# Kernel optimization log

Hardware: AMD Instinct MI355X
Metric: run time of the kernel (lower is better)

## Reference

```python
import jax, jax.numpy as jnp
import numpy as np

DIM = 384
HEAD_DIM = 32
NUM_HEADS = DIM // HEAD_DIM
SCALE = HEAD_DIM ** -0.5


def setup_inputs() -> dict:
    key = jax.random.key(0)
    k1, k2, k3, k4 = jax.random.split(key, 4)
    x = jax.random.normal(k1, (8, DIM, 32, 32), dtype=jnp.float32)
    # torch nn.Linear stores weight as [out_features, in_features]
    W_qkv = jax.random.normal(k2, (3 * DIM, DIM), dtype=jnp.float32) * (DIM ** -0.5)
    W_proj = jax.random.normal(k3, (DIM, DIM), dtype=jnp.float32) * (DIM ** -0.5)
    b_proj = jax.random.normal(k4, (DIM,), dtype=jnp.float32) * 0.01
    return {"x": x, "W_qkv": W_qkv, "W_proj": W_proj, "b_proj": b_proj}


def reference(x, W_qkv, W_proj, b_proj):
    B, C, H, W = x.shape
    N = H * W
    # flatten spatial -> tokens: (B, N, C)
    xt = x.reshape(B, C, N).transpose(0, 2, 1)
    # qkv projection (no bias): (B, N, 3C)
    qkv = jnp.einsum('bnc,oc->bno', xt, W_qkv)
    qkv = qkv.reshape(B, N, 3, NUM_HEADS, HEAD_DIM).transpose(2, 0, 3, 1, 4)
    q, k, v = qkv[0], qkv[1], qkv[2]  # each (B, h, N, d)
    attn = jnp.einsum('bhnd,bhmd->bhnm', q * SCALE, k)  # (B, h, N, N)
    attn = jax.nn.softmax(attn, axis=-1)
    out = jnp.einsum('bhnm,bhmd->bhnd', attn, v)  # (B, h, N, d)
    out = out.transpose(0, 2, 1, 3).reshape(B, N, C)
    out = jnp.einsum('bnc,oc->bno', out, W_proj) + b_proj
    # back to (B, C, H, W)
    return out.transpose(0, 2, 1).reshape(B, C, H, W)
```

## Files before the change

### kernel.cpp

```cpp
#include <hip/hip_runtime.h>
#include <hip/hip_bf16.h>

#define DIM   384
#define HD    32
#define NH    12
#define NT    1024
#define BATCH 8
#define C2 0.2550347244197545f
#define M2 11.541560327111707f


typedef short shortx8 __attribute__((ext_vector_type(8)));
typedef float floatx4 __attribute__((ext_vector_type(4)));

#define GLD_LDS(gp, lp) \
    __builtin_amdgcn_global_load_lds((__attribute__((address_space(1))) const void*)(gp), \
                                     (__attribute__((address_space(3))) void*)(lp), 16, 0, 0)

static __device__ __forceinline__ unsigned short f2bf(float f) {
    unsigned int u = __float_as_uint(f);
    u += 0x7fffu + ((u >> 16) & 1u);
    return (unsigned short)(u >> 16);
}

__global__ __launch_bounds__(256) void k_pre(const float* __restrict__ x,
                                             const float* __restrict__ wq,
                                             const float* __restrict__ wp,
                                             unsigned short* __restrict__ xtf,
                                             unsigned short* __restrict__ wqf,
                                             unsigned short* __restrict__ wpf) {
    const int bid = blockIdx.x;
    if (bid < 3072) {
        __shared__ float t[32][33];
        const int xb_ = bid & 31, kstep = (bid >> 5) % 12, b = bid / 384;
        const int n0 = xb_ * 32;
        const int tid = threadIdx.x;
        const int tx = tid & 31, ty = tid >> 5;
        const float* xb = x + ((size_t)b * DIM + kstep * 32) * NT + n0;
#pragma unroll
        for (int i = 0; i < 4; i++)
            t[ty + 8 * i][tx] = xb[(size_t)(ty + 8 * i) * NT + tx];
        __syncthreads();
        const int mtl = tid >> 7, kq = (tid >> 5) & 3, rem = tid & 31;
        const int mrow = rem >> 1, krH = rem & 1;
        ushort4 p;
        p.x = f2bf(t[kq * 8 + krH * 4 + 0][mtl * 16 + mrow]);
        p.y = f2bf(t[kq * 8 + krH * 4 + 1][mtl * 16 + mrow]);
        p.z = f2bf(t[kq * 8 + krH * 4 + 2][mtl * 16 + mrow]);
        p.w = f2bf(t[kq * 8 + krH * 4 + 3][mtl * 16 + mrow]);
        const size_t mtile = ((size_t)b * 1024 + n0) / 16 + mtl;
        const size_t off = ((mtile * 12 + kstep) * 4 + kq) * 128 + mrow * 8 + krH * 4;
        *(ushort4*)(xtf + off) = p;
    } else {
        const int tid = (bid - 3072) * 256 + threadIdx.x;
        const float* src; unsigned short* dst; int ci;
        if (tid < 110592) { ci = tid; src = wq; dst = wqf; }
        else              { ci = tid - 110592; src = wp; dst = wpf; }
        const int krH = ci & 1, orow = (ci >> 1) & 15, quad = (ci >> 5) & 3;
        const int t2 = ci >> 7, kstep = t2 % 12, ntile = t2 / 12;
        const int row = ntile * 16 + orow, col = kstep * 32 + quad * 8 + krH * 4;
        const float4 v = *(const float4*)(src + (size_t)row * DIM + col);
        ushort4 p;
        p.x = f2bf(v.x); p.y = f2bf(v.y); p.z = f2bf(v.z); p.w = f2bf(v.w);
        *(ushort4*)(dst + (size_t)ci * 4) = p;
    }
}

__global__ __launch_bounds__(256) void k_qkv(const unsigned short* __restrict__ xtf,
                                             const unsigned short* __restrict__ wqf,
                                             unsigned short* __restrict__ qb,
                                             unsigned short* __restrict__ kb,
                                             unsigned short* __restrict__ vt) {
    const int lane = threadIdx.x & 63, w = threadIdx.x >> 6;
    const int quad = lane >> 4, l16 = lane & 15;
    const int m0 = blockIdx.x * 128 + (w & 1) * 64;
    const int n0 = blockIdx.y * 128 + (w >> 1) * 64;
    floatx4 acc[4][4] = {};
    const unsigned short* abase = xtf + ((size_t)(m0 >> 4) * 12 * 4 + quad) * 128 + l16 * 8;
    const unsigned short* bbase = wqf + ((size_t)(n0 >> 4) * 12 * 4 + quad) * 128 + l16 * 8;
    shortx8 a[4], b[4], a2[4], b2[4];
#pragma unroll
    for (int s = 0; s < 4; s++) {
        a[s] = *(const shortx8*)(abase + s * 6144);
        b[s] = *(const shortx8*)(bbase + s * 6144);
    }
    for (int ks = 0; ks < 12; ks++) {
        if (ks < 11) {
#pragma unroll
            for (int s = 0; s < 4; s++) {
                a2[s] = *(const shortx8*)(abase + s * 6144 + (ks + 1) * 512);
                b2[s] = *(const shortx8*)(bbase + s * 6144 + (ks + 1) * 512);
            }
        }
#pragma unroll
        for (int sm = 0; sm < 4; sm++)
#pragma unroll
            for (int sn = 0; sn < 4; sn++)
                acc[sm][sn] = __builtin_amdgcn_mfma_f32_16x16x32_bf16(a[sm], b[sn], acc[sm][sn], 0, 0, 0);
#pragma unroll
        for (int s = 0; s < 4; s++) { a[s] = a2[s]; b[s] = b2[s]; }
    }
    const int bi = m0 >> 10;
#pragma unroll
    for (int sn = 0; sn < 4; sn++) {
        const int o = n0 + sn * 16 + l16;
        const int which = (o >= 2 * DIM) ? 2 : (o >= DIM ? 1 : 0);
        const int rem = o - which * DIM;
        const int h = rem >> 5, d = rem & 31;
        const int hi = bi * NH + h;
#pragma unroll
        for (int sm = 0; sm < 4; sm++) {
#pragma unroll
            for (int r = 0; r < 4; r++) {
                const int n = (m0 + sm * 16 + quad * 4 + r) & 1023;
                const unsigned short val = f2bf(acc[sm][sn][r]);
                if (which == 0)      qb[((size_t)hi * NT + n) * HD + d] = val;
                else if (which == 1) kb[((size_t)hi * NT + n) * HD + d] = val;
                else                 vt[((size_t)hi * HD + d) * NT + n] = val;
            }
        }
    }
}

__global__ __launch_bounds__(256) void k_attn(const unsigned short* __restrict__ qb,
                                              const unsigned short* __restrict__ kb,
                                              const unsigned short* __restrict__ vt,
                                              unsigned short* __restrict__ aoutf) {
    __shared__ __align__(16) unsigned short frag[2][4][512];
    const int lane = threadIdx.x & 63, w = threadIdx.x >> 6;
    const int quad = lane >> 4, l16 = lane & 15;
    const int g = blockIdx.x & 7, j = blockIdx.x >> 3;
    const int hi = g * 12 + j % 12;
    const int q0 = ((j / 12) * 4 + w) * 32;
    const unsigned short* Q = qb + (size_t)hi * NT * HD;
    const unsigned short* K = kb + (size_t)hi * NT * HD;
    const unsigned short* V = vt + (size_t)hi * HD * NT;

    const shortx8 qfA = *(const shortx8*)(Q + (size_t)(q0 + l16) * HD + quad * 8);
    const shortx8 qfB = *(const shortx8*)(Q + (size_t)(q0 + 16 + l16) * HD + quad * 8);
    const int krow = (l16 >> 2) * 8 + (l16 & 3);
    const unsigned short* gsrc0;
    if (w == 0)      gsrc0 = K + (size_t)krow * HD + quad * 8;
    else if (w == 1) gsrc0 = K + (size_t)(krow + 4) * HD + quad * 8;
    else if (w == 2) gsrc0 = V + (size_t)l16 * NT + quad * 8;
    else             gsrc0 = V + (size_t)(16 + l16) * NT + quad * 8;
    const int gstep = (w < 2) ? 32 * HD : 32;

    const shortx8 ones = {16256, 16256, 16256, 16256, 16256, 16256, 16256, 16256};
    floatx4 oloA = {}, ohiA = {}, dsA = {};
    floatx4 oloB = {}, ohiB = {}, dsB = {};
    const floatx4 zero = {};

    GLD_LDS(gsrc0, &frag[0][w][0]);
    __syncthreads();

    for (int t = 0; t < 32; t++) {
        if (t < 31) GLD_LDS(gsrc0 + (size_t)(t + 1) * gstep, &frag[(t + 1) & 1][w][0]);
        const unsigned short* fb = &frag[t & 1][0][0];
        const shortx8 kf0 = *(const shortx8*)(fb + 0 * 512 + lane * 8);
        const shortx8 kf1 = *(const shortx8*)(fb + 1 * 512 + lane * 8);
        const shortx8 vlo = *(const shortx8*)(fb + 2 * 512 + lane * 8);
        const shortx8 vhi = *(const shortx8*)(fb + 3 * 512 + lane * 8);
        const floatx4 sA0 = __builtin_amdgcn_mfma_f32_16x16x32_bf16(kf0, qfA, zero, 0, 0, 0);
        const floatx4 sA1 = __builtin_amdgcn_mfma_f32_16x16x32_bf16(kf1, qfA, zero, 0, 0, 0);
        const floatx4 sB0 = __builtin_amdgcn_mfma_f32_16x16x32_bf16(kf0, qfB, zero, 0, 0, 0);
        const floatx4 sB1 = __builtin_amdgcn_mfma_f32_16x16x32_bf16(kf1, qfB, zero, 0, 0, 0);
        float eA[8], eB[8];
#pragma unroll
        for (int r = 0; r < 4; r++) {
            eA[r]     = __builtin_amdgcn_exp2f(fmaf(sA0[r], C2, -M2));
            eA[4 + r] = __builtin_amdgcn_exp2f(fmaf(sA1[r], C2, -M2));
            eB[r]     = __builtin_amdgcn_exp2f(fmaf(sB0[r], C2, -M2));
            eB[4 + r] = __builtin_amdgcn_exp2f(fmaf(sB1[r], C2, -M2));
        }
        union { shortx8 s8; __hip_bfloat162 h[4]; } pA, pB;
#pragma unroll
        for (int i = 0; i < 4; i++) {
            pA.h[i] = __float22bfloat162_rn(make_float2(eA[2 * i], eA[2 * i + 1]));
            pB.h[i] = __float22bfloat162_rn(make_float2(eB[2 * i], eB[2 * i + 1]));
        }
        oloA = __builtin_amdgcn_mfma_f32_16x16x32_bf16(pA.s8, vlo, oloA, 0, 0, 0);
        ohiA = __builtin_amdgcn_mfma_f32_16x16x32_bf16(pA.s8, vhi, ohiA, 0, 0, 0);
        dsA  = __builtin_amdgcn_mfma_f32_16x16x32_bf16(pA.s8, ones, dsA, 0, 0, 0);
        oloB = __builtin_amdgcn_mfma_f32_16x16x32_bf16(pB.s8, vlo, oloB, 0, 0, 0);
        ohiB = __builtin_amdgcn_mfma_f32_16x16x32_bf16(pB.s8, vhi, ohiB, 0, 0, 0);
        dsB  = __builtin_amdgcn_mfma_f32_16x16x32_bf16(pB.s8, ones, dsB, 0, 0, 0);
        __syncthreads();
    }
    const int bi = hi / NH, h = hi % NH;
    const size_t mt0 = (size_t)bi * 64 + (q0 >> 4);
    const int kqlo = l16 >> 3, kr = l16 & 7;
    unsigned short* pAp = aoutf + (mt0 * 12 + h) * 512 + kr;
    unsigned short* pBp = aoutf + ((mt0 + 1) * 12 + h) * 512 + kr;
#pragma unroll
    for (int r = 0; r < 4; r++) {
        const int mrow8 = (quad * 4 + r) * 8;
        const float invA = 1.0f / dsA[r], invB = 1.0f / dsB[r];
        pAp[kqlo * 128 + mrow8]       = f2bf(oloA[r] * invA);
        pAp[(2 + kqlo) * 128 + mrow8] = f2bf(ohiA[r] * invA);
        pBp[kqlo * 128 + mrow8]       = f2bf(oloB[r] * invB);
        pBp[(2 + kqlo) * 128 + mrow8] = f2bf(ohiB[r] * invB);
    }
}

__global__ __launch_bounds__(256) void k_proj(const unsigned short* __restrict__ aoutf,
                                              const unsigned short* __restrict__ wpf,
                                              const float* __restrict__ bias,
                                              float* __restrict__ out) {
    const int lane = threadIdx.x & 63, w = threadIdx.x >> 6;
    const int quad = lane >> 4, l16 = lane & 15;
    const int m0 = blockIdx.x * 128 + (w & 1) * 64;
    const int n0 = blockIdx.y * 128 + (w >> 1) * 64;
    floatx4 acc[4][4] = {};
    const unsigned short* abase = aoutf + ((size_t)(m0 >> 4) * 12 * 4 + quad) * 128 + l16 * 8;
    const unsigned short* bbase = wpf + ((size_t)(n0 >> 4) * 12 * 4 + quad) * 128 + l16 * 8;
    shortx8 a[4], b[4], a2[4], b2[4];
#pragma unroll
    for (int s = 0; s < 4; s++) {
        a[s] = *(const shortx8*)(abase + s * 6144);
        b[s] = *(const shortx8*)(bbase + s * 6144);
    }
    for (int ks = 0; ks < 12; ks++) {
        if (ks < 11) {
#pragma unroll
            for (int s = 0; s < 4; s++) {
                a2[s] = *(const shortx8*)(abase + s * 6144 + (ks + 1) * 512);
                b2[s] = *(const shortx8*)(bbase + s * 6144 + (ks + 1) * 512);
            }
        }
#pragma unroll
        for (int sm = 0; sm < 4; sm++)
#pragma unroll
            for (int sn = 0; sn < 4; sn++)
                acc[sm][sn] = __builtin_amdgcn_mfma_f32_16x16x32_bf16(a[sm], b[sn], acc[sm][sn], 0, 0, 0);
#pragma unroll
        for (int s = 0; s < 4; s++) { a[s] = a2[s]; b[s] = b2[s]; }
    }
    const int bi = m0 >> 10;
#pragma unroll
    for (int sn = 0; sn < 4; sn++) {
        const int o = n0 + sn * 16 + l16;
        const float bv = bias[o];
        float* orow = out + ((size_t)bi * DIM + o) * NT;
#pragma unroll
        for (int sm = 0; sm < 4; sm++) {
            const int nb = (m0 + sm * 16 + quad * 4) & 1023;
            float4 pack;
            pack.x = acc[sm][sn][0] + bv;
            pack.y = acc[sm][sn][1] + bv;
            pack.z = acc[sm][sn][2] + bv;
            pack.w = acc[sm][sn][3] + bv;
            *(float4*)(orow + nb) = pack;
        }
    }
}

extern "C" void kernel_launch(void* const* d_in, const int* in_sizes, int n_in,
                              void* d_out, int out_size, void* d_ws, size_t ws_size,
                              hipStream_t stream) {
    const float* x     = (const float*)d_in[0];
    const float* wqkv  = (const float*)d_in[1];
    const float* wproj = (const float*)d_in[2];
    const float* bias  = (const float*)d_in[3];
    float* out = (float*)d_out;

    unsigned short* xtf  = (unsigned short*)d_ws;
    unsigned short* qb   = xtf + 3145728;
    unsigned short* kb   = qb + 3145728;
    unsigned short* vt   = kb + 3145728;
    unsigned short* wqf  = vt + 3145728;
    unsigned short* wpf  = wqf + 442368;
    unsigned short* aoutf = xtf;

    k_pre<<<3648, 256, 0, stream>>>(x, wqkv, wproj, xtf, wqf, wpf);
    k_qkv<<<dim3(64, 9), 256, 0, stream>>>(xtf, wqf, qb, kb, vt);
    k_attn<<<768, 256, 0, stream>>>(qb, kb, vt, aoutf);
    k_proj<<<dim3(64, 3), 256, 0, stream>>>(aoutf, wpf, bias, out);
}
```

Measured before the change: 128.6 us.

## Deepen GEMM prefetch, batch attention KV tiles, and retile projection grid

The QKV and projection GEMMs now prefetch two k-steps ahead using triple-buffered register fragments instead of one, and both declare a two-blocks-per-CU launch bound. The attention kernel stages eight K/V tiles per LDS phase, so it synchronises four times instead of thirty-two while keeping a double buffer. The projection kernel uses smaller 64x128 block tiles with twice as many blocks to fill more CUs. These changes aim to hide load latency and cut barrier overhead, at the cost of more registers and 64KB of LDS per attention block, which may lower occupancy.

Result: no change. 131.0 us (+1.8%).

```diff
diff --git a/kernel.cpp b/kernel.cpp
--- a/kernel.cpp
+++ b/kernel.cpp
@@ -21,6 +21,25 @@
     unsigned int u = __float_as_uint(f);
     u += 0x7fffu + ((u >> 16) & 1u);
     return (unsigned short)(u >> 16);
+}
+
+template <int NA, int NB>
+static __device__ __forceinline__ void ldfrag(shortx8 (&A)[NA], shortx8 (&B)[NB],
+                                              const unsigned short* ab,
+                                              const unsigned short* bb, int ks) {
+#pragma unroll
+    for (int s = 0; s < NA; s++) A[s] = *(const shortx8*)(ab + s * 6144 + ks * 512);
+#pragma unroll
+    for (int s = 0; s < NB; s++) B[s] = *(const shortx8*)(bb + s * 6144 + ks * 512);
+}
+template <int NA, int NB>
+static __device__ __forceinline__ void mmblk(floatx4 (&acc)[NA][NB],
+                                             const shortx8 (&A)[NA], const shortx8 (&B)[NB]) {
+#pragma unroll
+    for (int sm = 0; sm < NA; sm++)
+#pragma unroll
+        for (int sn = 0; sn < NB; sn++)
+            acc[sm][sn] = __builtin_amdgcn_mfma_f32_16x16x32_bf16(A[sm], B[sn], acc[sm][sn], 0, 0, 0);
 }
 
 __global__ __launch_bounds__(256) void k_pre(const float* __restrict__ x,
@@ -66,11 +85,11 @@
     }
 }
 
-__global__ __launch_bounds__(256) void k_qkv(const unsigned short* __restrict__ xtf,
-                                             const unsigned short* __restrict__ wqf,
-                                             unsigned short* __restrict__ qb,
-                                             unsigned short* __restrict__ kb,
-                                             unsigned short* __restrict__ vt) {
+__global__ __launch_bounds__(256, 2) void k_qkv(const unsigned short* __restrict__ xtf,
+                                                const unsigned short* __restrict__ wqf,
+                                                unsigned short* __restrict__ qb,
+                                                unsigned short* __restrict__ kb,
+                                                unsigned short* __restrict__ vt) {
     const int lane = threadIdx.x & 63, w = threadIdx.x >> 6;
     const int quad = lane >> 4, l16 = lane & 15;
     const int m0 = blockIdx.x * 128 + (w & 1) * 64;
@@ -78,27 +97,17 @@
     floatx4 acc[4][4] = {};
     const unsigned short* abase = xtf + ((size_t)(m0 >> 4) * 12 * 4 + quad) * 128 + l16 * 8;
     const unsigned short* bbase = wqf + ((size_t)(n0 >> 4) * 12 * 4 + quad) * 128 + l16 * 8;
-    shortx8 a[4], b[4], a2[4], b2[4];
-#pragma unroll
-    for (int s = 0; s < 4; s++) {
-        a[s] = *(const shortx8*)(abase + s * 6144);
-        b[s] = *(const shortx8*)(bbase + s * 6144);
-    }
-    for (int ks = 0; ks < 12; ks++) {
-        if (ks < 11) {
-#pragma unroll
-            for (int s = 0; s < 4; s++) {
-                a2[s] = *(const shortx8*)(abase + s * 6144 + (ks + 1) * 512);
-                b2[s] = *(const shortx8*)(bbase + s * 6144 + (ks + 1) * 512);
-            }
-        }
-#pragma unroll
-        for (int sm = 0; sm < 4; sm++)
-#pragma unroll
-            for (int sn = 0; sn < 4; sn++)
-                acc[sm][sn] = __builtin_amdgcn_mfma_f32_16x16x32_bf16(a[sm], b[sn], acc[sm][sn], 0, 0, 0);
-#pragma unroll
-        for (int s = 0; s < 4; s++) { a[s] = a2[s]; b[s] = b2[s]; }
+    shortx8 A0[4], B0[4], A1[4], B1[4], A2[4], B2[4];
+    ldfrag(A0, B0, abase, bbase, 0);
+    ldfrag(A1, B1, abase, bbase, 1);
+#pragma unroll
+    for (int ks = 0; ks < 12; ks += 3) {
+        if (ks + 2 < 12) ldfrag(A2, B2, abase, bbase, ks + 2);
+        mmblk(acc, A0, B0);
+        if (ks + 3 < 12) ldfrag(A0, B0, abase, bbase, ks + 3);
+        mmblk(acc, A1, B1);
+        if (ks + 4 < 12) ldfrag(A1, B1, abase, bbase, ks + 4);
+        mmblk(acc, A2, B2);
     }
     const int bi = m0 >> 10;
 #pragma unroll
@@ -126,7 +135,7 @@
                                               const unsigned short* __restrict__ kb,
                                               const unsigned short* __restrict__ vt,
                                               unsigned short* __restrict__ aoutf) {
-    __shared__ __align__(16) unsigned short frag[2][4][512];
+    __shared__ __align__(16) unsigned short frag[2][8][4][512];
     const int lane = threadIdx.x & 63, w = threadIdx.x >> 6;
     const int quad = lane >> 4, l16 = lane & 15;
     const int g = blockIdx.x & 7, j = blockIdx.x >> 3;
@@ -151,40 +160,50 @@
     floatx4 oloB = {}, ohiB = {}, dsB = {};
     const floatx4 zero = {};
 
-    GLD_LDS(gsrc0, &frag[0][w][0]);
+#pragma unroll
+    for (int t = 0; t < 8; t++)
+        GLD_LDS(gsrc0 + (size_t)t * gstep, &frag[0][t][w][0]);
     __syncthreads();
 
-    for (int t = 0; t < 32; t++) {
-        if (t < 31) GLD_LDS(gsrc0 + (size_t)(t + 1) * gstep, &frag[(t + 1) & 1][w][0]);
-        const unsigned short* fb = &frag[t & 1][0][0];
-        const shortx8 kf0 = *(const shortx8*)(fb + 0 * 512 + lane * 8);
-        const shortx8 kf1 = *(const shortx8*)(fb + 1 * 512 + lane * 8);
-        const shortx8 vlo = *(const shortx8*)(fb + 2 * 512 + lane * 8);
-        const shortx8 vhi = *(const shortx8*)(fb + 3 * 512 + lane * 8);
-        const floatx4 sA0 = __builtin_amdgcn_mfma_f32_16x16x32_bf16(kf0, qfA, zero, 0, 0, 0);
-        const floatx4 sA1 = __builtin_amdgcn_mfma_f32_16x16x32_bf16(kf1, qfA, zero, 0, 0, 0);
-        const floatx4 sB0 = __builtin_amdgcn_mfma_f32_16x16x32_bf16(kf0, qfB, zero, 0, 0, 0);
-        const floatx4 sB1 = __builtin_amdgcn_mfma_f32_16x16x32_bf16(kf1, qfB, zero, 0, 0, 0);
-        float eA[8], eB[8];
-#pragma unroll
-        for (int r = 0; r < 4; r++) {
-            eA[r]     = __builtin_amdgcn_exp2f(fmaf(sA0[r], C2, -M2));
-            eA[4 + r] = __builtin_amdgcn_exp2f(fmaf(sA1[r], C2, -M2));
-            eB[r]     = __builtin_amdgcn_exp2f(fmaf(sB0[r], C2, -M2));
-            eB[4 + r] = __builtin_amdgcn_exp2f(fmaf(sB1[r], C2, -M2));
-        }
-        union { shortx8 s8; __hip_bfloat162 h[4]; } pA, pB;
-#pragma unroll
-        for (int i = 0; i < 4; i++) {
-            pA.h[i] = __float22bfloat162_rn(make_float2(eA[2 * i], eA[2 * i + 1]));
-            pB.h[i] = __float22bfloat162_rn(make_float2(eB[2 * i], eB[2 * i + 1]));
-        }
-        oloA = __builtin_amdgcn_mfma_f32_16x16x32_bf16(pA.s8, vlo, oloA, 0, 0, 0);
-        ohiA = __builtin_amdgcn_mfma_f32_16x16x32_bf16(pA.s8, vhi, ohiA, 0, 0, 0);
-        dsA  = __builtin_amdgcn_mfma_f32_16x16x32_bf16(pA.s8, ones, dsA, 0, 0, 0);
-        oloB = __builtin_amdgcn_mfma_f32_16x16x32_bf16(pB.s8, vlo, oloB, 0, 0, 0);
-        ohiB = __builtin_amdgcn_mfma_f32_16x16x32_bf16(pB.s8, vhi, ohiB, 0, 0, 0);
-        dsB  = __builtin_amdgcn_mfma_f32_16x16x32_bf16(pB.s8, ones, dsB, 0, 0, 0);
+    for (int p = 0; p < 4; p++) {
+        const int pb = p & 1;
+        if (p < 3) {
+#pragma unroll
+            for (int t = 0; t < 8; t++)
+                GLD_LDS(gsrc0 + (size_t)((p + 1) * 8 + t) * gstep, &frag[pb ^ 1][t][w][0]);
+        }
+#pragma unroll
+        for (int t = 0; t < 8; t++) {
+            const unsigned short* fb = &frag[pb][t][0][0];
+            const shortx8 kf0 = *(const shortx8*)(fb + 0 * 512 + lane * 8);
+            const shortx8 kf1 = *(const shortx8*)(fb + 1 * 512 + lane * 8);
+            const shortx8 vlo = *(const shortx8*)(fb + 2 * 512 + lane * 8);
+            const shortx8 vhi = *(const shortx8*)(fb + 3 * 512 + lane * 8);
+            const floatx4 sA0 = __builtin_amdgcn_mfma_f32_16x16x32_bf16(kf0, qfA, zero, 0, 0, 0);
+            const floatx4 sA1 = __builtin_amdgcn_mfma_f32_16x16x32_bf16(kf1, qfA, zero, 0, 0, 0);
+            const floatx4 sB0 = __builtin_amdgcn_mfma_f32_16x16x32_bf16(kf0, qfB, zero, 0, 0, 0);
+            const floatx4 sB1 = __builtin_amdgcn_mfma_f32_16x16x32_bf16(kf1, qfB, zero, 0, 0, 0);
+            float eA[8], eB[8];
+#pragma unroll
+            for (int r = 0; r < 4; r++) {
+                eA[r]     = __builtin_amdgcn_exp2f(fmaf(sA0[r], C2, -M2));
+                eA[4 + r] = __builtin_amdgcn_exp2f(fmaf(sA1[r], C2, -M2));
+                eB[r]     = __builtin_amdgcn_exp2f(fmaf(sB0[r], C2, -M2));
+                eB[4 + r] = __builtin_amdgcn_exp2f(fmaf(sB1[r], C2, -M2));
+            }
+            union { shortx8 s8; __hip_bfloat162 h[4]; } pA, pB;
+#pragma unroll
+            for (int i = 0; i < 4; i++) {
+                pA.h[i] = __float22bfloat162_rn(make_float2(eA[2 * i], eA[2 * i + 1]));
+                pB.h[i] = __float22bfloat162_rn(make_float2(eB[2 * i], eB[2 * i + 1]));
+            }
+            oloA = __builtin_amdgcn_mfma_f32_16x16x32_bf16(pA.s8, vlo, oloA, 0, 0, 0);
+            ohiA = __builtin_amdgcn_mfma_f32_16x16x32_bf16(pA.s8, vhi, ohiA, 0, 0, 0);
+            dsA  = __builtin_amdgcn_mfma_f32_16x16x32_bf16(pA.s8, ones, dsA, 0, 0, 0);
+            oloB = __builtin_amdgcn_mfma_f32_16x16x32_bf16(pB.s8, vlo, oloB, 0, 0, 0);
+            ohiB = __builtin_amdgcn_mfma_f32_16x16x32_bf16(pB.s8, vhi, ohiB, 0, 0, 0);
+            dsB  = __builtin_amdgcn_mfma_f32_16x16x32_bf16(pB.s8, ones, dsB, 0, 0, 0);
+        }
         __syncthreads();
     }
     const int bi = hi / NH, h = hi % NH;
@@ -203,42 +222,32 @@
     }
 }
 
-__global__ __launch_bounds__(256) void k_proj(const unsigned short* __restrict__ aoutf,
-                                              const unsigned short* __restrict__ wpf,
-                                              const float* __restrict__ bias,
-                                              float* __restrict__ out) {
+__global__ __launch_bounds__(256, 2) void k_proj(const unsigned short* __restrict__ aoutf,
+                                                 const unsigned short* __restrict__ wpf,
+                                                 const float* __restrict__ bias,
+                                                 float* __restrict__ out) {
     const int lane = threadIdx.x & 63, w = threadIdx.x >> 6;
     const int quad = lane >> 4, l16 = lane & 15;
-    const int m0 = blockIdx.x * 128 + (w & 1) * 64;
-    const int n0 = blockIdx.y * 128 + (w >> 1) * 64;
-    floatx4 acc[4][4] = {};
+    const int m0 = blockIdx.x * 64;
+    const int n0 = blockIdx.y * 128 + w * 32;
+    floatx4 acc[4][2] = {};
     const unsigned short* abase = aoutf + ((size_t)(m0 >> 4) * 12 * 4 + quad) * 128 + l16 * 8;
     const unsigned short* bbase = wpf + ((size_t)(n0 >> 4) * 12 * 4 + quad) * 128 + l16 * 8;
-    shortx8 a[4], b[4], a2[4], b2[4];
-#pragma unroll
-    for (int s = 0; s < 4; s++) {
-        a[s] = *(const shortx8*)(abase + s * 6144);
-        b[s] = *(const shortx8*)(bbase + s * 6144);
-    }
-    for (int ks = 0; ks < 12; ks++) {
-        if (ks < 11) {
-#pragma unroll
-            for (int s = 0; s < 4; s++) {
-                a2[s] = *(const shortx8*)(abase + s * 6144 + (ks + 1) * 512);
-                b2[s] = *(const shortx8*)(bbase + s * 6144 + (ks + 1) * 512);
-            }
-        }
-#pragma unroll
-        for (int sm = 0; sm < 4; sm++)
-#pragma unroll
-            for (int sn = 0; sn < 4; sn++)
-                acc[sm][sn] = __builtin_amdgcn_mfma_f32_16x16x32_bf16(a[sm], b[sn], acc[sm][sn], 0, 0, 0);
-#pragma unroll
-        for (int s = 0; s < 4; s++) { a[s] = a2[s]; b[s] = b2[s]; }
+    shortx8 A0[4], B0[2], A1[4], B1[2], A2[4], B2[2];
+    ldfrag(A0, B0, abase, bbase, 0);
+    ldfrag(A1, B1, abase, bbase, 1);
+#pragma unroll
+    for (int ks = 0; ks < 12; ks += 3) {
+        if (ks + 2 < 12) ldfrag(A2, B2, abase, bbase, ks + 2);
+        mmblk(acc, A0, B0);
+        if (ks + 3 < 12) ldfrag(A0, B0, abase, bbase, ks + 3);
+        mmblk(acc, A1, B1);
+        if (ks + 4 < 12) ldfrag(A1, B1, abase, bbase, ks + 4);
+        mmblk(acc, A2, B2);
     }
     const int bi = m0 >> 10;
 #pragma unroll
-    for (int sn = 0; sn < 4; sn++) {
+    for (int sn = 0; sn < 2; sn++) {
         const int o = n0 + sn * 16 + l16;
         const float bv = bias[o];
         float* orow = out + ((size_t)bi * DIM + o) * NT;
@@ -275,5 +284,5 @@
     k_pre<<<3648, 256, 0, stream>>>(x, wqkv, wproj, xtf, wqf, wpf);
     k_qkv<<<dim3(64, 9), 256, 0, stream>>>(xtf, wqf, qb, kb, vt);
     k_attn<<<768, 256, 0, stream>>>(qb, kb, vt, aoutf);
-    k_proj<<<dim3(64, 3), 256, 0, stream>>>(aoutf, wpf, bias, out);
-}
+    k_proj<<<dim3(128, 3), 256, 0, stream>>>(aoutf, wpf, bias, out);
+}
```
